# Optimization experiments

Hardware: AMD Instinct MI355X
Metric: run time of the kernel (lower is better)

## Reference

```python
import jax, jax.numpy as jnp
import numpy as np

SIGMA = 1.0


def _rbf_gram(A, B):
    # A: (Tb, N, C), B: (Tb, M, C) -> (Tb, N, M)
    AA = jnp.sum(A * A, axis=2, keepdims=True)          # (Tb, N, 1)
    BB = jnp.sum(B * B, axis=2, keepdims=True)          # (Tb, M, 1)
    d = AA + jnp.swapaxes(BB, 1, 2) - 2.0 * jnp.einsum('bnc,bmc->bnm', A, B)
    return jnp.exp(-d / (2.0 * SIGMA ** 2))


def setup_inputs() -> dict:
    key = jax.random.key(0)
    kx, ky = jax.random.split(key)
    x = jax.random.normal(kx, (512, 128, 16), dtype=jnp.float32)
    y = jax.random.normal(ky, (512, 128, 16), dtype=jnp.float32)
    return {"x": x, "y": y}


def reference(x, y):
    # x, y: (batch, stream, channel)
    x_fds = jnp.concatenate((x[:, :-1, :], x[:, 1:, :]), axis=1)  # (B, 2(T-1), C)
    y_fds = jnp.concatenate((y[:, :-1, :], y[:, 1:, :]), axis=1)
    xf = jnp.transpose(x_fds, (1, 0, 2))  # (2(T-1), B, C)
    yf = jnp.transpose(y_fds, (1, 0, 2))

    N = xf.shape[1]
    Kxx = _rbf_gram(xf, xf)  # (2(T-1), N, N)
    # off-diagonal mean per batch: (sum - trace) / (N*(N-1))
    e_xx = (Kxx.sum(axis=(1, 2)) - jnp.trace(Kxx, axis1=1, axis2=2)) / (N * (N - 1))
    E_k_x1_x2 = e_xx.mean()

    Kxy = _rbf_gram(xf, yf)
    E_k_x_y = Kxy.mean(axis=(1, 2)).mean()

    return E_k_x1_x2 - 2.0 * E_k_x_y
```

## Files before the change

kernel.cpp:

```cpp
#include <hip/hip_runtime.h>


#define LOG2E 1.4426950408889634f
#define SCALE 1.2011224087864498f

typedef __attribute__((ext_vector_type(8))) __bf16 bf16x8;
typedef __attribute__((ext_vector_type(4))) float floatx4;

union FragU { uint4 q; unsigned int u[4]; bf16x8 v; };

static __device__ __forceinline__ int off(int n) { return (n << 3) + ((n >> 2) << 2); }

static __device__ __forceinline__ unsigned short bfbits(__bf16 h) {
    union { __bf16 h; unsigned short s; } u; u.h = h; return u.s;
}
static __device__ __forceinline__ unsigned int packhh(__bf16 a, __bf16 b) {
    return (unsigned int)bfbits(a) | ((unsigned int)bfbits(b) << 16);
}

__global__ __launch_bounds__(256, 4) void gram_kernel(const float* __restrict__ x,
                                                      const float* __restrict__ y,
                                                      float* __restrict__ part) {
    __shared__ unsigned int XH[1152], XL[1152], YH[1152], YL[1152];
    __shared__ float csx[128], csy[128];
    __shared__ float srg[256];
    __shared__ float red[8];

    const int bid   = blockIdx.x;
    const int t     = bid >> 3;
    const int strip = (bid >> 2) & 1;
    const int jq    = bid & 3;
    const int tid   = threadIdx.x;
    const int w     = tid >> 6;
    const int lane  = tid & 63;
    const int quad  = lane >> 4;
    const int l15   = lane & 15;
    const int qh    = quad & 1;

    const float4* __restrict__ x4 = (const float4*)x;
    const float4* __restrict__ y4 = (const float4*)y;
    const int slab4 = t * 4;

    {
        const int half = tid >> 7;
        const int n    = tid & 127;
        const float4* __restrict__ src4 = half ? y4 : x4;
        const size_t gb = (size_t)(jq * 128 + n) * 512 + slab4;
        float4 f0 = src4[gb], f1 = src4[gb + 1], f2 = src4[gb + 2], f3 = src4[gb + 3];
        float fs[16] = { f0.x, f0.y, f0.z, f0.w, f1.x, f1.y, f1.z, f1.w,
                         f2.x, f2.y, f2.z, f2.w, f3.x, f3.y, f3.z, f3.w };
        float g = 0.f;
        unsigned int hw[8], lw[8];
#pragma unroll
        for (int p = 0; p < 8; ++p) {
            float s0 = fs[2 * p] * SCALE, s1 = fs[2 * p + 1] * SCALE;
            g += fs[2 * p] * fs[2 * p] + fs[2 * p + 1] * fs[2 * p + 1];
            __bf16 h0 = (__bf16)s0, h1 = (__bf16)s1;
            hw[p] = packhh(h0, h1);
            lw[p] = packhh((__bf16)(s0 - (float)h0), (__bf16)(s1 - (float)h1));
        }
        unsigned int* __restrict__ H = half ? YH : XH;
        unsigned int* __restrict__ L = half ? YL : XL;
        const int o = off(n);
        *(uint4*)&H[o]     = make_uint4(hw[0], hw[1], hw[2], hw[3]);
        *(uint4*)&H[o + 4] = make_uint4(hw[4], hw[5], hw[6], hw[7]);
        *(uint4*)&L[o]     = make_uint4(lw[0], lw[1], lw[2], lw[3]);
        *(uint4*)&L[o + 4] = make_uint4(lw[4], lw[5], lw[6], lw[7]);
        float* cs = half ? csy : csx;
        cs[n] = __builtin_amdgcn_exp2f(-0.5f * LOG2E * g);
    }
    {
        const size_t gb = (size_t)(strip * 256 + tid) * 512 + slab4;
        float4 f0 = x4[gb], f1 = x4[gb + 1], f2 = x4[gb + 2], f3 = x4[gb + 3];
        float g = f0.x * f0.x + f0.y * f0.y + f0.z * f0.z + f0.w * f0.w
                + f1.x * f1.x + f1.y * f1.y + f1.z * f1.z + f1.w * f1.w
                + f2.x * f2.x + f2.y * f2.y + f2.z * f2.z + f2.w * f2.w
                + f3.x * f3.x + f3.y * f3.y + f3.z * f3.z + f3.w * f3.w;
        srg[tid] = 0.5f * LOG2E * g;
    }

    bf16x8 a1f[4], a2f[4];
    {
        bf16x8 zv;
#pragma unroll
        for (int j = 0; j < 8; ++j) zv[j] = (__bf16)0.0f;
#pragma unroll
        for (int rt = 0; rt < 4; ++rt) {
            const int row = strip * 256 + w * 64 + rt * 16 + l15;
            const size_t gb = (size_t)row * 512 + slab4 + qh * 2;
            float4 f0 = x4[gb], f1 = x4[gb + 1];
            float sc[8] = { f0.x * SCALE, f0.y * SCALE, f0.z * SCALE, f0.w * SCALE,
                            f1.x * SCALE, f1.y * SCALE, f1.z * SCALE, f1.w * SCALE };
            bf16x8 hv, lv;
#pragma unroll
            for (int j = 0; j < 8; ++j) {
                __bf16 h = (__bf16)sc[j];
                hv[j] = h;
                lv[j] = (__bf16)(sc[j] - (float)h);
            }
            a1f[rt] = (quad < 2) ? hv : lv;
            a2f[rt] = (quad < 2) ? hv : zv;
        }
    }
    __syncthreads();

    float sxx[4][4], sxy[4][4];
#pragma unroll
    for (int rt = 0; rt < 4; ++rt)
#pragma unroll
        for (int r = 0; r < 4; ++r) { sxx[rt][r] = 0.f; sxy[rt][r] = 0.f; }

    for (int jt = 0; jt < 8; ++jt) {
        const int n  = jt * 16 + l15;
        const int rb = off(n) + qh * 4;
        FragU bh, bl, ch, cl;
        bh.q = *(const uint4*)&XH[rb];
        bl.q = *(const uint4*)&XL[rb];
        ch.q = *(const uint4*)&YH[rb];
        cl.q = *(const uint4*)&YL[rb];
        const float cx = csx[n];
        const float cy = csy[n];
#pragma unroll
        for (int rt = 0; rt < 4; ++rt) {
            floatx4 c = {0.f, 0.f, 0.f, 0.f};
            c = __builtin_amdgcn_mfma_f32_16x16x32_bf16(a1f[rt], bh.v, c, 0, 0, 0);
            c = __builtin_amdgcn_mfma_f32_16x16x32_bf16(a2f[rt], bl.v, c, 0, 0, 0);
#pragma unroll
            for (int r = 0; r < 4; ++r)
                sxx[rt][r] = fmaf(__builtin_amdgcn_exp2f(c[r]), cx, sxx[rt][r]);
            floatx4 d = {0.f, 0.f, 0.f, 0.f};
            d = __builtin_amdgcn_mfma_f32_16x16x32_bf16(a1f[rt], ch.v, d, 0, 0, 0);
            d = __builtin_amdgcn_mfma_f32_16x16x32_bf16(a2f[rt], cl.v, d, 0, 0, 0);
#pragma unroll
            for (int r = 0; r < 4; ++r)
                sxy[rt][r] = fmaf(__builtin_amdgcn_exp2f(d[r]), cy, sxy[rt][r]);
        }
    }

    float txx = 0.f, txy = 0.f;
#pragma unroll
    for (int rt = 0; rt < 4; ++rt)
#pragma unroll
        for (int r = 0; r < 4; ++r) {
            const float rs = __builtin_amdgcn_exp2f(-srg[w * 64 + rt * 16 + quad * 4 + r]);
            txx = fmaf(sxx[rt][r], rs, txx);
            txy = fmaf(sxy[rt][r], rs, txy);
        }
    for (int o = 32; o > 0; o >>= 1) {
        txx += __shfl_down(txx, o, 64);
        txy += __shfl_down(txy, o, 64);
    }
    if (lane == 0) { red[w] = txx; red[4 + w] = txy; }
    __syncthreads();
    if (tid == 0) {
        const float wt = (t == 0 || t == 127) ? 1.f : 2.f;
        part[bid]        = wt * (red[0] + red[1] + red[2] + red[3]);
        part[1024 + bid] = wt * (red[4] + red[5] + red[6] + red[7]);
    }
}

__global__ __launch_bounds__(256) void finalize_kernel(const float* __restrict__ part,
                                                       float* __restrict__ out) {
    const int tid = threadIdx.x;
    double vxx = 0.0, vxy = 0.0;
#pragma unroll
    for (int k = 0; k < 4; ++k) {
        vxx += (double)part[tid + 256 * k];
        vxy += (double)part[1024 + tid + 256 * k];
    }
    for (int o = 32; o > 0; o >>= 1) {
        vxx += __shfl_down(vxx, o, 64);
        vxy += __shfl_down(vxy, o, 64);
    }
    __shared__ double red[8];
    const int wid = tid >> 6;
    if ((tid & 63) == 0) { red[wid] = vxx; red[4 + wid] = vxy; }
    __syncthreads();
    if (tid == 0) {
        double sxx = red[0] + red[1] + red[2] + red[3];
        double sxy = red[4] + red[5] + red[6] + red[7];
        double e1 = (sxx - 254.0 * 512.0) / (254.0 * 512.0 * 511.0);
        double e2 = sxy / (254.0 * 512.0 * 512.0);
        out[0] = (float)(e1 - 2.0 * e2);
    }
}

extern "C" void kernel_launch(void* const* d_in, const int* in_sizes, int n_in,
                              void* d_out, int out_size, void* d_ws, size_t ws_size,
                              hipStream_t stream) {
    (void)in_sizes; (void)n_in; (void)out_size; (void)ws_size;
    const float* x = (const float*)d_in[0];
    const float* y = (const float*)d_in[1];
    float* out  = (float*)d_out;
    float* part = (float*)d_ws;

    gram_kernel<<<dim3(1024), dim3(256), 0, stream>>>(x, y, part);
    finalize_kernel<<<dim3(1), dim3(256), 0, stream>>>(part, out);
}
```

Measured before the change: 77.51 us.

## Precompute bf16 hi/lo splits and norms in a separate prep kernel

```diff
diff --git a/kernel.cpp b/kernel.cpp
--- a/kernel.cpp
+++ b/kernel.cpp
@@ -4,6 +4,15 @@
 #define LOG2E 1.4426950408889634f
 #define SCALE 1.2011224087864498f
 
+#define XH_OFF   0u
+#define XL_OFF   524288u
+#define YH_OFF   1048576u
+#define YL_OFF   1572864u
+#define GX_OFF   2097152u
+#define CSX_OFF  2162688u
+#define CSY_OFF  2228224u
+#define PART_OFF 2293760u
+
 typedef __attribute__((ext_vector_type(8))) __bf16 bf16x8;
 typedef __attribute__((ext_vector_type(4))) float floatx4;
 
@@ -18,10 +27,46 @@
     return (unsigned int)bfbits(a) | ((unsigned int)bfbits(b) << 16);
 }
 
-__global__ __launch_bounds__(256, 4) void gram_kernel(const float* __restrict__ x,
-                                                      const float* __restrict__ y,
+__global__ __launch_bounds__(256) void prep_kernel(const float* __restrict__ x,
+                                                   const float* __restrict__ y,
+                                                   unsigned int* __restrict__ ws) {
+    const int bid = blockIdx.x, tid = threadIdx.x;
+    const int m   = bid >> 8;
+    const int t   = (bid >> 1) & 127;
+    const int row = ((bid & 1) << 8) + tid;
+
+    const float4* __restrict__ src4 = m ? (const float4*)y : (const float4*)x;
+    const size_t gb = (size_t)row * 512 + t * 4;
+    float4 f0 = src4[gb], f1 = src4[gb + 1], f2 = src4[gb + 2], f3 = src4[gb + 3];
+    const float fs[16] = { f0.x, f0.y, f0.z, f0.w, f1.x, f1.y, f1.z, f1.w,
+                           f2.x, f2.y, f2.z, f2.w, f3.x, f3.y, f3.z, f3.w };
+    float g = 0.f;
+    unsigned int hw[8], lw[8];
+#pragma unroll
+    for (int p = 0; p < 8; ++p) {
+        const float v0 = fs[2 * p], v1 = fs[2 * p + 1];
+        g += v0 * v0 + v1 * v1;
+        const float s0 = v0 * SCALE, s1 = v1 * SCALE;
+        const __bf16 h0 = (__bf16)s0, h1 = (__bf16)s1;
+        hw[p] = packhh(h0, h1);
+        lw[p] = packhh((__bf16)(s0 - (float)h0), (__bf16)(s1 - (float)h1));
+    }
+    const float gp = 0.5f * LOG2E * g;
+    const unsigned int idx = (unsigned int)t * 512u + (unsigned int)row;
+    unsigned int* __restrict__ H = ws + (m ? YH_OFF : XH_OFF) + (size_t)idx * 8;
+    unsigned int* __restrict__ L = ws + (m ? YL_OFF : XL_OFF) + (size_t)idx * 8;
+    *(uint4*)&H[0] = make_uint4(hw[0], hw[1], hw[2], hw[3]);
+    *(uint4*)&H[4] = make_uint4(hw[4], hw[5], hw[6], hw[7]);
+    *(uint4*)&L[0] = make_uint4(lw[0], lw[1], lw[2], lw[3]);
+    *(uint4*)&L[4] = make_uint4(lw[4], lw[5], lw[6], lw[7]);
+    float* __restrict__ wsf = (float*)ws;
+    wsf[(m ? CSY_OFF : CSX_OFF) + idx] = __builtin_amdgcn_exp2f(-gp);
+    if (!m) wsf[GX_OFF + idx] = gp;
+}
+
+__global__ __launch_bounds__(256, 4) void gram_kernel(const unsigned int* __restrict__ ws,
                                                       float* __restrict__ part) {
-    __shared__ unsigned int XH[1152], XL[1152], YH[1152], YL[1152];
+    __shared__ unsigned int XHs[1152], XLs[1152], YHs[1152], YLs[1152];
     __shared__ float csx[128], csy[128];
     __shared__ float srg[256];
     __shared__ float red[8];
@@ -36,70 +81,42 @@
     const int quad  = lane >> 4;
     const int l15   = lane & 15;
     const int qh    = quad & 1;
-
-    const float4* __restrict__ x4 = (const float4*)x;
-    const float4* __restrict__ y4 = (const float4*)y;
-    const int slab4 = t * 4;
+    const float* __restrict__ wsf = (const float*)ws;
 
     {
-        const int half = tid >> 7;
-        const int n    = tid & 127;
-        const float4* __restrict__ src4 = half ? y4 : x4;
-        const size_t gb = (size_t)(jq * 128 + n) * 512 + slab4;
-        float4 f0 = src4[gb], f1 = src4[gb + 1], f2 = src4[gb + 2], f3 = src4[gb + 3];
-        float fs[16] = { f0.x, f0.y, f0.z, f0.w, f1.x, f1.y, f1.z, f1.w,
-                         f2.x, f2.y, f2.z, f2.w, f3.x, f3.y, f3.z, f3.w };
-        float g = 0.f;
-        unsigned int hw[8], lw[8];
-#pragma unroll
-        for (int p = 0; p < 8; ++p) {
-            float s0 = fs[2 * p] * SCALE, s1 = fs[2 * p + 1] * SCALE;
-            g += fs[2 * p] * fs[2 * p] + fs[2 * p + 1] * fs[2 * p + 1];
-            __bf16 h0 = (__bf16)s0, h1 = (__bf16)s1;
-            hw[p] = packhh(h0, h1);
-            lw[p] = packhh((__bf16)(s0 - (float)h0), (__bf16)(s1 - (float)h1));
-        }
-        unsigned int* __restrict__ H = half ? YH : XH;
-        unsigned int* __restrict__ L = half ? YL : XL;
-        const int o = off(n);
-        *(uint4*)&H[o]     = make_uint4(hw[0], hw[1], hw[2], hw[3]);
-        *(uint4*)&H[o + 4] = make_uint4(hw[4], hw[5], hw[6], hw[7]);
-        *(uint4*)&L[o]     = make_uint4(lw[0], lw[1], lw[2], lw[3]);
-        *(uint4*)&L[o + 4] = make_uint4(lw[4], lw[5], lw[6], lw[7]);
-        float* cs = half ? csy : csx;
-        cs[n] = __builtin_amdgcn_exp2f(-0.5f * LOG2E * g);
-    }
-    {
-        const size_t gb = (size_t)(strip * 256 + tid) * 512 + slab4;
-        float4 f0 = x4[gb], f1 = x4[gb + 1], f2 = x4[gb + 2], f3 = x4[gb + 3];
-        float g = f0.x * f0.x + f0.y * f0.y + f0.z * f0.z + f0.w * f0.w
-                + f1.x * f1.x + f1.y * f1.y + f1.z * f1.z + f1.w * f1.w
-                + f2.x * f2.x + f2.y * f2.y + f2.z * f2.z + f2.w * f2.w
-                + f3.x * f3.x + f3.y * f3.y + f3.z * f3.z + f3.w * f3.w;
-        srg[tid] = 0.5f * LOG2E * g;
-    }
+        const int a = tid >> 6, idx = tid & 63;
+        const unsigned int abase = (a == 0) ? XH_OFF : (a == 1) ? XL_OFF
+                                 : (a == 2) ? YH_OFF : YL_OFF;
+        const unsigned int* __restrict__ gsrc =
+            ws + abase + ((size_t)t * 512 + jq * 128) * 8 + (size_t)idx * 16;
+        uint4 q0 = *(const uint4*)&gsrc[0];
+        uint4 q1 = *(const uint4*)&gsrc[4];
+        uint4 q2 = *(const uint4*)&gsrc[8];
+        uint4 q3 = *(const uint4*)&gsrc[12];
+        unsigned int* __restrict__ dst = (a == 0) ? XHs : (a == 1) ? XLs
+                                       : (a == 2) ? YHs : YLs;
+        const int r0 = idx * 2;
+        *(uint4*)&dst[off(r0)]         = q0;
+        *(uint4*)&dst[off(r0) + 4]     = q1;
+        *(uint4*)&dst[off(r0 + 1)]     = q2;
+        *(uint4*)&dst[off(r0 + 1) + 4] = q3;
+    }
+    if (tid < 128) csx[tid]       = wsf[CSX_OFF + t * 512 + jq * 128 + tid];
+    else           csy[tid - 128] = wsf[CSY_OFF + t * 512 + jq * 128 + (tid - 128)];
+    srg[tid] = wsf[GX_OFF + t * 512 + strip * 256 + tid];
 
     bf16x8 a1f[4], a2f[4];
     {
-        bf16x8 zv;
-#pragma unroll
-        for (int j = 0; j < 8; ++j) zv[j] = (__bf16)0.0f;
+        FragU z; z.q = make_uint4(0u, 0u, 0u, 0u);
+        const unsigned int hbase = (quad < 2) ? XH_OFF : XL_OFF;
 #pragma unroll
         for (int rt = 0; rt < 4; ++rt) {
             const int row = strip * 256 + w * 64 + rt * 16 + l15;
-            const size_t gb = (size_t)row * 512 + slab4 + qh * 2;
-            float4 f0 = x4[gb], f1 = x4[gb + 1];
-            float sc[8] = { f0.x * SCALE, f0.y * SCALE, f0.z * SCALE, f0.w * SCALE,
-                            f1.x * SCALE, f1.y * SCALE, f1.z * SCALE, f1.w * SCALE };
-            bf16x8 hv, lv;
-#pragma unroll
-            for (int j = 0; j < 8; ++j) {
-                __bf16 h = (__bf16)sc[j];
-                hv[j] = h;
-                lv[j] = (__bf16)(sc[j] - (float)h);
-            }
-            a1f[rt] = (quad < 2) ? hv : lv;
-            a2f[rt] = (quad < 2) ? hv : zv;
+            const unsigned int* __restrict__ p =
+                ws + hbase + ((size_t)t * 512 + row) * 8 + qh * 4;
+            FragU u; u.q = *(const uint4*)p;
+            a1f[rt] = u.v;
+            a2f[rt] = (quad < 2) ? u.v : z.v;
         }
     }
     __syncthreads();
@@ -114,10 +131,10 @@
         const int n  = jt * 16 + l15;
         const int rb = off(n) + qh * 4;
         FragU bh, bl, ch, cl;
-        bh.q = *(const uint4*)&XH[rb];
-        bl.q = *(const uint4*)&XL[rb];
-        ch.q = *(const uint4*)&YH[rb];
-        cl.q = *(const uint4*)&YL[rb];
+        bh.q = *(const uint4*)&XHs[rb];
+        bl.q = *(const uint4*)&XLs[rb];
+        ch.q = *(const uint4*)&YHs[rb];
+        cl.q = *(const uint4*)&YLs[rb];
         const float cx = csx[n];
         const float cy = csy[n];
 #pragma unroll
@@ -191,9 +208,11 @@
     (void)in_sizes; (void)n_in; (void)out_size; (void)ws_size;
     const float* x = (const float*)d_in[0];
     const float* y = (const float*)d_in[1];
-    float* out  = (float*)d_out;
-    float* part = (float*)d_ws;
-
-    gram_kernel<<<dim3(1024), dim3(256), 0, stream>>>(x, y, part);
+    float* out = (float*)d_out;
+    unsigned int* ws = (unsigned int*)d_ws;
+    float* part = (float*)d_ws + PART_OFF;
+
+    prep_kernel<<<dim3(512), dim3(256), 0, stream>>>(x, y, ws);
+    gram_kernel<<<dim3(1024), dim3(256), 0, stream>>>(ws, part);
     finalize_kernel<<<dim3(1), dim3(256), 0, stream>>>(part, out);
 }
```

New measurement: 79.63 us. 1.03x slower.
